# Optimization experiments

Measured on AMD Instinct MI355X. Metric: run time of the kernel, lower is better.

## Reference

```python
import jax, jax.numpy as jnp
import numpy as np

N_AA = 20
A = 15
D_FEAT = 128
CA_IDX = 1
NUM_FUNCS = 3
FREQ_BANDS = jnp.array([1.0, 2.0, 3.0, 1.0, 0.5, 1.0 / 3.0], dtype=jnp.float32)


def setup_inputs() -> dict:
    key = jax.random.key(0)
    ks = jax.random.split(key, 16)
    b, L = 16, 1024
    d_in = D_FEAT + N_AA * A * 3 + 3 * (NUM_FUNCS * 2 * 2 + 1) + D_FEAT  # 1195
    inp = {
        "seq": jax.random.randint(ks[0], (b, L), 0, N_AA),
        "xyz": jax.random.normal(ks[1], (b, L, A, 3), dtype=jnp.float32),
        "dihedrals": jax.random.normal(ks[2], (b, L, 3), dtype=jnp.float32),
        "chain_idx": jax.random.randint(ks[3], (b, L), 0, 10),
        "orientation": jax.random.normal(ks[4], (b, L, 3, 3), dtype=jnp.float32),
        "atom_mask": jnp.ones((b, L, A), dtype=bool),
        "aa_emb": jax.random.normal(ks[5], (N_AA, D_FEAT), dtype=jnp.float32),
        "chain_emb": jax.random.normal(ks[6], (10, D_FEAT), dtype=jnp.float32).at[0].set(0.0),  # padding_idx=0
        "W1": jax.random.normal(ks[7], (d_in, 2 * D_FEAT), dtype=jnp.float32) * 0.02,
        "b1": jnp.zeros((2 * D_FEAT,), dtype=jnp.float32),
        "W2": jax.random.normal(ks[8], (2 * D_FEAT, D_FEAT), dtype=jnp.float32) * 0.02,
        "b2": jnp.zeros((D_FEAT,), dtype=jnp.float32),
        "W3": jax.random.normal(ks[9], (D_FEAT, D_FEAT), dtype=jnp.float32) * 0.02,
        "b3": jnp.zeros((D_FEAT,), dtype=jnp.float32),
        "W4": jax.random.normal(ks[10], (D_FEAT, D_FEAT), dtype=jnp.float32) * 0.02,
        "b4": jnp.zeros((D_FEAT,), dtype=jnp.float32),
    }
    return inp


def angular_encoding(x):
    # x: (..., d_in) -> (..., d_in * 13)
    xe = x[..., None]  # (..., d_in, 1)
    enc = jnp.concatenate([xe, jnp.sin(FREQ_BANDS * xe), jnp.cos(FREQ_BANDS * xe)], axis=-1)
    return enc.reshape(*x.shape[:-1], -1)


def reference(seq, xyz, dihedrals, chain_idx, orientation, atom_mask,
              aa_emb, chain_emb, W1, b1, W2, b2, W3, b3, W4, b4):
    b, L = seq.shape
    aa_type_feat = aa_emb[seq]  # (b, L, d_feat)

    # local coordinates relative to CA, rotated into local frame via O^T
    xyz_rel = xyz - xyz[:, :, CA_IDX:CA_IDX + 1, :]  # (b, L, A, 3)
    xyz_local = jnp.einsum('blji,blaj->blai', orientation, xyz_rel)  # O^T @ xyz_rel

    # one-hot select: place xyz_local in the slot of the residue's aa type
    onehot = jax.nn.one_hot(seq, N_AA, dtype=xyz.dtype)  # (b, L, 20)
    coord_feat = (onehot[:, :, :, None, None] * xyz_local[:, :, None, :, :]).reshape(b, L, N_AA * A * 3)

    dihedral_feat = angular_encoding(dihedrals)  # (b, L, 39)

    chain_feat = chain_emb[chain_idx] * (chain_idx != 0)[..., None].astype(xyz.dtype)  # padding_idx=0

    x = jnp.concatenate([aa_type_feat, coord_feat, dihedral_feat, chain_feat], axis=-1)
    h = jax.nn.relu(x @ W1 + b1)
    h = jax.nn.relu(h @ W2 + b2)
    h = jax.nn.relu(h @ W3 + b3)
    return h @ W4 + b4
```

## Files before the change

### kernel.cpp

```cpp
#include <hip/hip_runtime.h>
#include <math.h>

#define N_AA    20
#define NATOM   15
#define TM      32
#define MAXBL   16384
#define MAXBLK  (MAXBL / TM + N_AA)
#define NWAVE   16

#define FSX  104
#define HSX  264
#define H2SX 136

typedef __attribute__((ext_vector_type(8))) short bf16x8;
typedef __attribute__((ext_vector_type(4))) float f32x4;

#define W1F_SLOTS  (N_AA * 16 * 3 * 64)
#define W2F_SLOTS  (8 * 8 * 64)
#define W34F_SLOTS (8 * 4 * 64)
#define TOT_SLOTS  (W1F_SLOTS + W2F_SLOTS + 2 * W34F_SLOTS)

__device__ __forceinline__ unsigned short f2bf(float x) {
    unsigned u = __float_as_uint(x);
    return (unsigned short)((u + 0x7FFFu + ((u >> 16) & 1u)) >> 16);
}
__device__ __forceinline__ float bf2f(unsigned short h) {
    return __uint_as_float(((unsigned)h) << 16);
}
__device__ __forceinline__ void put2(unsigned short* H, unsigned short* L, int idx, float v) {
    unsigned short hi = f2bf(v);
    H[idx] = hi;
    L[idx] = f2bf(v - bf2f(hi));
}

__global__ __launch_bounds__(1024) void prep_kernel(
    const int* __restrict__ seq, const float* __restrict__ aa_emb,
    const float* __restrict__ chain_emb, const float* __restrict__ W1,
    const float* __restrict__ W2, const float* __restrict__ W3, const float* __restrict__ W4,
    int BL,
    float* __restrict__ aaT, float* __restrict__ chT,
    int* __restrict__ bucket_start, int* __restrict__ blk_type,
    int* __restrict__ blk_chunk, int* __restrict__ rowidx,
    unsigned short* __restrict__ W1fH, unsigned short* __restrict__ W1fL,
    unsigned short* __restrict__ W2fH, unsigned short* __restrict__ W2fL,
    unsigned short* __restrict__ W3fH, unsigned short* __restrict__ W3fL,
    unsigned short* __restrict__ W4fH, unsigned short* __restrict__ W4fL)
{
    const int t = threadIdx.x;
    const int b = blockIdx.x;

    if (b < 8) {
        const int tab = b * 4 + (t >> 8);
        const int col = t & 255;
        if (tab < 30) {
            if (tab < N_AA) {
                const float* e = aa_emb + tab * 128;
                float acc = 0.f;
                #pragma unroll 8
                for (int k = 0; k < 128; ++k)
                    acc += e[k] * W1[(size_t)k * 256 + col];
                aaT[tab * 256 + col] = acc;
            } else {
                const int c = tab - N_AA;
                const float* e = chain_emb + c * 128;
                float acc = 0.f;
                #pragma unroll 8
                for (int k = 0; k < 128; ++k)
                    acc += e[k] * W1[(size_t)(1067 + k) * 256 + col];
                chT[c * 256 + col] = acc;
            }
        }
        return;
    }

    if (b >= 9) {
        const int slot = (b - 9) * 1024 + t;
        if (slot >= TOT_SLOTS) return;
        float v[8];
        unsigned short *dH, *dL;
        if (slot < W1F_SLOTS) {
            const int g = slot / 3072, r1 = slot % 3072;
            const int tile = r1 / 192, chunk = (r1 / 64) % 3, lane = r1 % 64;
            const int n  = tile * 16 + (lane & 15);
            const int kb = chunk * 32 + (lane >> 4) * 8;
            #pragma unroll
            for (int j = 0; j < 8; ++j) {
                const int k = kb + j;
                float x = 0.f;
                if (k < 45)       x = W1[(size_t)(128 + g * 45 + k) * 256 + n];
                else if (k < 84)  x = W1[(size_t)(1028 + k - 45) * 256 + n];
                v[j] = x;
            }
            dH = W1fH + (size_t)slot * 8; dL = W1fL + (size_t)slot * 8;
        } else if (slot < W1F_SLOTS + W2F_SLOTS) {
            const int s = slot - W1F_SLOTS;
            const int tile = s / 512, chunk = (s / 64) % 8, lane = s % 64;
            const int n  = tile * 16 + (lane & 15);
            const int kb = chunk * 32 + (lane >> 4) * 8;
            #pragma unroll
            for (int j = 0; j < 8; ++j) v[j] = W2[(size_t)(kb + j) * 128 + n];
            dH = W2fH + (size_t)s * 8; dL = W2fL + (size_t)s * 8;
        } else if (slot < W1F_SLOTS + W2F_SLOTS + W34F_SLOTS) {
            const int s = slot - W1F_SLOTS - W2F_SLOTS;
            const int tile = s / 256, chunk = (s / 64) % 4, lane = s % 64;
            const int n  = tile * 16 + (lane & 15);
            const int kb = chunk * 32 + (lane >> 4) * 8;
            #pragma unroll
            for (int j = 0; j < 8; ++j) v[j] = W3[(size_t)(kb + j) * 128 + n];
            dH = W3fH + (size_t)s * 8; dL = W3fL + (size_t)s * 8;
        } else {
            const int s = slot - W1F_SLOTS - W2F_SLOTS - W34F_SLOTS;
            const int tile = s / 256, chunk = (s / 64) % 4, lane = s % 64;
            const int n  = tile * 16 + (lane & 15);
            const int kb = chunk * 32 + (lane >> 4) * 8;
            #pragma unroll
            for (int j = 0; j < 8; ++j) v[j] = W4[(size_t)(kb + j) * 128 + n];
            dH = W4fH + (size_t)s * 8; dL = W4fL + (size_t)s * 8;
        }
        #pragma unroll
        for (int j = 0; j < 8; ++j) {
            const unsigned short hi = f2bf(v[j]);
            dH[j] = hi;
            dL[j] = f2bf(v[j] - bf2f(hi));
        }
        return;
    }

    __shared__ int sseq[MAXBL];
    __shared__ int hist[NWAVE][N_AA];
    __shared__ int wcur[NWAVE][N_AA];
    __shared__ int bs[N_AA + 1];
    __shared__ int blkoff[N_AA + 1];

    const int w = t >> 6;
    for (int i = t; i < BL; i += 1024) sseq[i] = seq[i];
    if (t < NWAVE * N_AA) hist[t / N_AA][t % N_AA] = 0;
    __syncthreads();
    for (int i = t; i < BL; i += 1024) atomicAdd(&hist[w][sseq[i]], 1);
    __syncthreads();
    if (t == 0) {
        int runr = 0, runb = 0;
        for (int g = 0; g < N_AA; ++g) {
            int s = 0;
            #pragma unroll
            for (int ww = 0; ww < NWAVE; ++ww) s += hist[ww][g];
            bs[g] = runr; runr += s;
            blkoff[g] = runb; runb += (s + TM - 1) / TM;
        }
        bs[N_AA] = runr; blkoff[N_AA] = runb;
    }
    __syncthreads();
    if (t <= N_AA) bucket_start[t] = bs[t];
    if (t < NWAVE * N_AA) {
        const int w2 = t / N_AA, g2 = t % N_AA;
        int o = bs[g2];
        for (int ww = 0; ww < w2; ++ww) o += hist[ww][g2];
        wcur[w2][g2] = o;
    }
    const int nblk = blkoff[N_AA];
    for (int i = t; i < MAXBLK; i += 1024) {
        if (i < nblk) {
            int g = 0;
            while (blkoff[g + 1] <= i) ++g;
            blk_type[i]  = g;
            blk_chunk[i] = i - blkoff[g];
        } else blk_type[i] = -1;
    }
    __syncthreads();
    for (int i = t; i < BL; i += 1024) {
        const int pos = atomicAdd(&wcur[w][sseq[i]], 1);
        rowidx[pos] = i;
    }
}

__global__ __launch_bounds__(256, 3) void fused_kernel(
    const int* __restrict__ chain_idx, const float* __restrict__ xyz,
    const float* __restrict__ dihedrals, const float* __restrict__ orientation,
    const float* __restrict__ b1, const float* __restrict__ b2,
    const float* __restrict__ b3, const float* __restrict__ b4,
    const float* __restrict__ aaT, const float* __restrict__ chT,
    const int* __restrict__ bucket_start, const int* __restrict__ blk_type,
    const int* __restrict__ blk_chunk, const int* __restrict__ rowidx,
    const unsigned short* __restrict__ W1fH, const unsigned short* __restrict__ W1fL,
    const unsigned short* __restrict__ W2fH, const unsigned short* __restrict__ W2fL,
    const unsigned short* __restrict__ W3fH, const unsigned short* __restrict__ W3fL,
    const unsigned short* __restrict__ W4fH, const unsigned short* __restrict__ W4fL,
    float* __restrict__ out)
{
    __shared__ __align__(16) unsigned short smemA[2 * TM * HSX];
    __shared__ __align__(16) unsigned short smemB[2 * TM * H2SX];
    __shared__ int s_row[TM], s_rowld[TM], s_chain[TM];

    unsigned short* hAH   = smemA;
    unsigned short* hAL   = smemA + TM * HSX;
    unsigned short* featH = smemB;
    unsigned short* featL = smemB + TM * FSX;
    unsigned short* hBH   = smemB;
    unsigned short* hBL   = smemB + TM * H2SX;

    const int t = threadIdx.x;

    const int nwg = gridDim.x;
    const int q = nwg >> 3, r = nwg & 7;
    const int xcd = blockIdx.x & 7, loc = blockIdx.x >> 3;
    const int bid = (xcd < r ? xcd * (q + 1) : r * (q + 1) + (xcd - r) * q) + loc;

    const int g = blk_type[bid];
    if (g < 0) return;
    const int chunk  = blk_chunk[bid];
    const int bstart = bucket_start[g] + chunk * TM;
    const int nrows  = min(TM, bucket_start[g + 1] - bstart);

    const int wave = t >> 6, lane = t & 63, quad = lane >> 4, nid = lane & 15;

    bf16x8 p1H[4], p1L[4];
    #pragma unroll
    for (int tt = 0; tt < 4; ++tt) {
        const size_t off = ((size_t)((g * 16 + (wave * 4 + tt)) * 3 + 0) * 64 + lane) * 8;
        p1H[tt] = *(const bf16x8*)(W1fH + off);
        p1L[tt] = *(const bf16x8*)(W1fL + off);
    }

    if (t < TM) {
        const bool valid = (t < nrows);
        const int rl = rowidx[valid ? (bstart + t) : bstart];
        s_row[t]   = valid ? rl : -1;
        s_rowld[t] = rl;
        s_chain[t] = chain_idx[rl];
    }
    __syncthreads();

    for (int i = t; i < TM * NATOM; i += 256) {
        const int rr = i / NATOM, a = i % NATOM;
        const int rl = s_rowld[rr];
        const float* xr = xyz + (size_t)rl * (NATOM * 3);
        const float cax = xr[3], cay = xr[4], caz = xr[5];
        const float rx = xr[a*3+0] - cax;
        const float ry = xr[a*3+1] - cay;
        const float rz = xr[a*3+2] - caz;
        const float* O = orientation + (size_t)rl * 9;
        put2(featH, featL, rr * FSX + a*3 + 0, O[0]*rx + O[3]*ry + O[6]*rz);
        put2(featH, featL, rr * FSX + a*3 + 1, O[1]*rx + O[4]*ry + O[7]*rz);
        put2(featH, featL, rr * FSX + a*3 + 2, O[2]*rx + O[5]*ry + O[8]*rz);
    }
    if (t < TM * 3) {
        const int rr = t / 3, d = t % 3;
        const float x = dihedrals[(size_t)s_rowld[rr] * 3 + d];
        const int base = rr * FSX + 45 + d * 13;
        const float F3 = (float)(1.0 / 3.0);
        const float s1 = sinf(x), c1 = cosf(x);
        put2(featH, featL, base + 0, x);
        put2(featH, featL, base + 1, s1);           put2(featH, featL, base + 2, sinf(2.f*x));
        put2(featH, featL, base + 3, sinf(3.f*x));  put2(featH, featL, base + 4, s1);
        put2(featH, featL, base + 5, sinf(0.5f*x)); put2(featH, featL, base + 6, sinf(F3*x));
        put2(featH, featL, base + 7, c1);           put2(featH, featL, base + 8, cosf(2.f*x));
        put2(featH, featL, base + 9, cosf(3.f*x));  put2(featH, featL, base +10, c1);
        put2(featH, featL, base +11, cosf(0.5f*x)); put2(featH, featL, base +12, cosf(F3*x));
    }
    if (t < TM) {
        #pragma unroll
        for (int k = 84; k < 96; ++k) { featH[t * FSX + k] = 0; featL[t * FSX + k] = 0; }
    }
    __syncthreads();

    const f32x4 zero = {0.f, 0.f, 0.f, 0.f};

    bf16x8 p2H[2], p2L[2];
    {
        f32x4 acc[2][4] = {{zero, zero, zero, zero}, {zero, zero, zero, zero}};
        #pragma unroll
        for (int c = 0; c < 3; ++c) {
            const bf16x8 aH0 = *(const bf16x8*)(featH + nid * FSX + c * 32 + quad * 8);
            const bf16x8 aL0 = *(const bf16x8*)(featL + nid * FSX + c * 32 + quad * 8);
            const bf16x8 aH1 = *(const bf16x8*)(featH + (16 + nid) * FSX + c * 32 + quad * 8);
            const bf16x8 aL1 = *(const bf16x8*)(featL + (16 + nid) * FSX + c * 32 + quad * 8);
            #pragma unroll
            for (int tt = 0; tt < 4; ++tt) {
                bf16x8 bH, bL;
                if (c == 0) { bH = p1H[tt]; bL = p1L[tt]; }
                else {
                    const size_t off = ((size_t)((g * 16 + (wave * 4 + tt)) * 3 + c) * 64 + lane) * 8;
                    bH = *(const bf16x8*)(W1fH + off);
                    bL = *(const bf16x8*)(W1fL + off);
                }
                acc[0][tt] = __builtin_amdgcn_mfma_f32_16x16x32_bf16(aH0, bH, acc[0][tt], 0, 0, 0);
                acc[0][tt] = __builtin_amdgcn_mfma_f32_16x16x32_bf16(aH0, bL, acc[0][tt], 0, 0, 0);
                acc[0][tt] = __builtin_amdgcn_mfma_f32_16x16x32_bf16(aL0, bH, acc[0][tt], 0, 0, 0);
                acc[1][tt] = __builtin_amdgcn_mfma_f32_16x16x32_bf16(aH1, bH, acc[1][tt], 0, 0, 0);
                acc[1][tt] = __builtin_amdgcn_mfma_f32_16x16x32_bf16(aH1, bL, acc[1][tt], 0, 0, 0);
                acc[1][tt] = __builtin_amdgcn_mfma_f32_16x16x32_bf16(aL1, bH, acc[1][tt], 0, 0, 0);
            }
        }
        #pragma unroll
        for (int tt = 0; tt < 2; ++tt) {
            const size_t off = ((size_t)((wave * 2 + tt) * 8 + 0) * 64 + lane) * 8;
            p2H[tt] = *(const bf16x8*)(W2fH + off);
            p2L[tt] = *(const bf16x8*)(W2fL + off);
        }
        #pragma unroll
        for (int tt = 0; tt < 4; ++tt) {
            const int j = (wave * 4 + tt) * 16 + nid;
            const float cb = b1[j] + aaT[g * 256 + j];
            #pragma unroll
            for (int rt = 0; rt < 2; ++rt) {
                #pragma unroll
                for (int rr = 0; rr < 4; ++rr) {
                    const int row = rt * 16 + quad * 4 + rr;
                    float v = acc[rt][tt][rr] + cb + chT[s_chain[row] * 256 + j];
                    v = fmaxf(v, 0.f);
                    put2(hAH, hAL, row * HSX + j, v);
                }
            }
        }
    }
    __syncthreads();

    bf16x8 p3H[2], p3L[2];
    {
        f32x4 acc[2][2] = {{zero, zero}, {zero, zero}};
        #pragma unroll
        for (int c = 0; c < 8; ++c) {
            const bf16x8 aH0 = *(const bf16x8*)(hAH + nid * HSX + c * 32 + quad * 8);
            const bf16x8 aL0 = *(const bf16x8*)(hAL + nid * HSX + c * 32 + quad * 8);
            const bf16x8 aH1 = *(const bf16x8*)(hAH + (16 + nid) * HSX + c * 32 + quad * 8);
            const bf16x8 aL1 = *(const bf16x8*)(hAL + (16 + nid) * HSX + c * 32 + quad * 8);
            #pragma unroll
            for (int tt = 0; tt < 2; ++tt) {
                bf16x8 bH, bL;
                if (c == 0) { bH = p2H[tt]; bL = p2L[tt]; }
                else {
                    const size_t off = ((size_t)((wave * 2 + tt) * 8 + c) * 64 + lane) * 8;
                    bH = *(const bf16x8*)(W2fH + off);
                    bL = *(const bf16x8*)(W2fL + off);
                }
                acc[0][tt] = __builtin_amdgcn_mfma_f32_16x16x32_bf16(aH0, bH, acc[0][tt], 0, 0, 0);
                acc[0][tt] = __builtin_amdgcn_mfma_f32_16x16x32_bf16(aH0, bL, acc[0][tt], 0, 0, 0);
                acc[0][tt] = __builtin_amdgcn_mfma_f32_16x16x32_bf16(aL0, bH, acc[0][tt], 0, 0, 0);
                acc[1][tt] = __builtin_amdgcn_mfma_f32_16x16x32_bf16(aH1, bH, acc[1][tt], 0, 0, 0);
                acc[1][tt] = __builtin_amdgcn_mfma_f32_16x16x32_bf16(aH1, bL, acc[1][tt], 0, 0, 0);
                acc[1][tt] = __builtin_amdgcn_mfma_f32_16x16x32_bf16(aL1, bH, acc[1][tt], 0, 0, 0);
            }
        }
        #pragma unroll
        for (int tt = 0; tt < 2; ++tt) {
            const size_t off = ((size_t)((wave * 2 + tt) * 4 + 0) * 64 + lane) * 8;
            p3H[tt] = *(const bf16x8*)(W3fH + off);
            p3L[tt] = *(const bf16x8*)(W3fL + off);
        }
        #pragma unroll
        for (int tt = 0; tt < 2; ++tt) {
            const int j = (wave * 2 + tt) * 16 + nid;
            const float bb = b2[j];
            #pragma unroll
            for (int rt = 0; rt < 2; ++rt) {
                #pragma unroll
                for (int rr = 0; rr < 4; ++rr) {
                    const int row = rt * 16 + quad * 4 + rr;
                    float v = fmaxf(acc[rt][tt][rr] + bb, 0.f);
                    put2(hBH, hBL, row * H2SX + j, v);
                }
            }
        }
    }
    __syncthreads();

    bf16x8 p4H[2], p4L[2];
    {
        f32x4 acc[2][2] = {{zero, zero}, {zero, zero}};
        #pragma unroll
        for (int c = 0; c < 4; ++c) {
            const bf16x8 aH0 = *(const bf16x8*)(hBH + nid * H2SX + c * 32 + quad * 8);
            const bf16x8 aL0 = *(const bf16x8*)(hBL + nid * H2SX + c * 32 + quad * 8);
            const bf16x8 aH1 = *(const bf16x8*)(hBH + (16 + nid) * H2SX + c * 32 + quad * 8);
            const bf16x8 aL1 = *(const bf16x8*)(hBL + (16 + nid) * H2SX + c * 32 + quad * 8);
            #pragma unroll
            for (int tt = 0; tt < 2; ++tt) {
                bf16x8 bH, bL;
                if (c == 0) { bH = p3H[tt]; bL = p3L[tt]; }
                else {
                    const size_t off = ((size_t)((wave * 2 + tt) * 4 + c) * 64 + lane) * 8;
                    bH = *(const bf16x8*)(W3fH + off);
                    bL = *(const bf16x8*)(W3fL + off);
                }
                acc[0][tt] = __builtin_amdgcn_mfma_f32_16x16x32_bf16(aH0, bH, acc[0][tt], 0, 0, 0);
                acc[0][tt] = __builtin_amdgcn_mfma_f32_16x16x32_bf16(aH0, bL, acc[0][tt], 0, 0, 0);
                acc[0][tt] = __builtin_amdgcn_mfma_f32_16x16x32_bf16(aL0, bH, acc[0][tt], 0, 0, 0);
                acc[1][tt] = __builtin_amdgcn_mfma_f32_16x16x32_bf16(aH1, bH, acc[1][tt], 0, 0, 0);
                acc[1][tt] = __builtin_amdgcn_mfma_f32_16x16x32_bf16(aH1, bL, acc[1][tt], 0, 0, 0);
                acc[1][tt] = __builtin_amdgcn_mfma_f32_16x16x32_bf16(aL1, bH, acc[1][tt], 0, 0, 0);
            }
        }
        #pragma unroll
        for (int tt = 0; tt < 2; ++tt) {
            const size_t off = ((size_t)((wave * 2 + tt) * 4 + 0) * 64 + lane) * 8;
            p4H[tt] = *(const bf16x8*)(W4fH + off);
            p4L[tt] = *(const bf16x8*)(W4fL + off);
        }
        #pragma unroll
        for (int tt = 0; tt < 2; ++tt) {
            const int j = (wave * 2 + tt) * 16 + nid;
            const float bb = b3[j];
            #pragma unroll
            for (int rt = 0; rt < 2; ++rt) {
                #pragma unroll
                for (int rr = 0; rr < 4; ++rr) {
                    const int row = rt * 16 + quad * 4 + rr;
                    float v = fmaxf(acc[rt][tt][rr] + bb, 0.f);
                    put2(hAH, hAL, row * HSX + j, v);
                }
            }
        }
    }
    __syncthreads();

    {
        f32x4 acc[2][2] = {{zero, zero}, {zero, zero}};
        #pragma unroll
        for (int c = 0; c < 4; ++c) {
            const bf16x8 aH0 = *(const bf16x8*)(hAH + nid * HSX + c * 32 + quad * 8);
            const bf16x8 aL0 = *(const bf16x8*)(hAL + nid * HSX + c * 32 + quad * 8);
            const bf16x8 aH1 = *(const bf16x8*)(hAH + (16 + nid) * HSX + c * 32 + quad * 8);
            const bf16x8 aL1 = *(const bf16x8*)(hAL + (16 + nid) * HSX + c * 32 + quad * 8);
            #pragma unroll
            for (int tt = 0; tt < 2; ++tt) {
                bf16x8 bH, bL;
                if (c == 0) { bH = p4H[tt]; bL = p4L[tt]; }
                else {
                    const size_t off = ((size_t)((wave * 2 + tt) * 4 + c) * 64 + lane) * 8;
                    bH = *(const bf16x8*)(W4fH + off);
                    bL = *(const bf16x8*)(W4fL + off);
                }
                acc[0][tt] = __builtin_amdgcn_mfma_f32_16x16x32_bf16(aH0, bH, acc[0][tt], 0, 0, 0);
                acc[0][tt] = __builtin_amdgcn_mfma_f32_16x16x32_bf16(aH0, bL, acc[0][tt], 0, 0, 0);
                acc[0][tt] = __builtin_amdgcn_mfma_f32_16x16x32_bf16(aL0, bH, acc[0][tt], 0, 0, 0);
                acc[1][tt] = __builtin_amdgcn_mfma_f32_16x16x32_bf16(aH1, bH, acc[1][tt], 0, 0, 0);
                acc[1][tt] = __builtin_amdgcn_mfma_f32_16x16x32_bf16(aH1, bL, acc[1][tt], 0, 0, 0);
                acc[1][tt] = __builtin_amdgcn_mfma_f32_16x16x32_bf16(aL1, bH, acc[1][tt], 0, 0, 0);
            }
        }
        #pragma unroll
        for (int tt = 0; tt < 2; ++tt) {
            const int j = (wave * 2 + tt) * 16 + nid;
            const float bb = b4[j];
            #pragma unroll
            for (int rt = 0; rt < 2; ++rt) {
                #pragma unroll
                for (int rr = 0; rr < 4; ++rr) {
                    const int row = rt * 16 + quad * 4 + rr;
                    const int orow = s_row[row];
                    if (orow >= 0) out[(size_t)orow * 128 + j] = acc[rt][tt][rr] + bb;
                }
            }
        }
    }
}

extern "C" void kernel_launch(void* const* d_in, const int* in_sizes, int n_in,
                              void* d_out, int out_size, void* d_ws, size_t ws_size,
                              hipStream_t stream) {
    const int*   seq    = (const int*)d_in[0];
    const float* xyz    = (const float*)d_in[1];
    const float* dihed  = (const float*)d_in[2];
    const int*   chain  = (const int*)d_in[3];
    const float* orient = (const float*)d_in[4];
    const float* aa_emb = (const float*)d_in[6];
    const float* ch_emb = (const float*)d_in[7];
    const float* W1 = (const float*)d_in[8];
    const float* b1 = (const float*)d_in[9];
    const float* W2 = (const float*)d_in[10];
    const float* b2 = (const float*)d_in[11];
    const float* W3 = (const float*)d_in[12];
    const float* b3 = (const float*)d_in[13];
    const float* W4 = (const float*)d_in[14];
    const float* b4 = (const float*)d_in[15];
    float* out = (float*)d_out;

    const int BL = in_sizes[0];

    char* p = (char*)d_ws;
    float* aaT = (float*)p;            p += 20 * 256 * 4;
    float* chT = (float*)p;            p += 10 * 256 * 4;
    int* bucket_start = (int*)p;       p += 32 * 4;
    int* blk_type     = (int*)p;       p += MAXBLK * 4;
    int* blk_chunk    = (int*)p;       p += MAXBLK * 4;
    int* rowidx       = (int*)p;       p += MAXBL * 4;
    p += ((16 - ((uintptr_t)p & 15)) & 15);
    unsigned short* W1fH = (unsigned short*)p; p += (size_t)W1F_SLOTS * 8 * 2;
    unsigned short* W1fL = (unsigned short*)p; p += (size_t)W1F_SLOTS * 8 * 2;
    unsigned short* W2fH = (unsigned short*)p; p += (size_t)W2F_SLOTS * 8 * 2;
    unsigned short* W2fL = (unsigned short*)p; p += (size_t)W2F_SLOTS * 8 * 2;
    unsigned short* W3fH = (unsigned short*)p; p += (size_t)W34F_SLOTS * 8 * 2;
    unsigned short* W3fL = (unsigned short*)p; p += (size_t)W34F_SLOTS * 8 * 2;
    unsigned short* W4fH = (unsigned short*)p; p += (size_t)W34F_SLOTS * 8 * 2;
    unsigned short* W4fL = (unsigned short*)p;

    const int nprep  = 9 + (TOT_SLOTS + 1023) / 1024;
    const int nfused = BL / TM + N_AA;

    prep_kernel<<<nprep, 1024, 0, stream>>>(seq, aa_emb, ch_emb, W1, W2, W3, W4, BL,
                                            aaT, chT, bucket_start, blk_type, blk_chunk, rowidx,
                                            W1fH, W1fL, W2fH, W2fL, W3fH, W3fL, W4fH, W4fL);
    fused_kernel<<<nfused, 256, 0, stream>>>(chain, xyz, dihed, orient,
                                             b1, b2, b3, b4, aaT, chT,
                                             bucket_start, blk_type, blk_chunk, rowidx,
                                             W1fH, W1fL, W2fH, W2fL, W3fH, W3fL, W4fH, W4fL,
                                             out);
}
```

Baseline: 121.6 us.

## Split residue bucket sort across sixteen blocks with inter-block flag synchronization

The counting sort that groups rows by amino-acid type used to run in one 1024-thread block. It is now spread over sixteen blocks. Each block histograms its own slice of rows and publishes the counts to global memory. The last block waits on per-block flags, builds the prefix offsets and block tables, then sets a ready flag, after which every block scatters its rows. This targets the serial bottleneck of one block scanning all rows inside the prep kernel. In exchange it relies on spin-waits that need all sixteen blocks resident at once. The flags are set to a magic value and never reset, so later calls can skip the waits and read stale or racing histograms.

```diff
diff --git a/kernel.cpp b/kernel.cpp
--- a/kernel.cpp
+++ b/kernel.cpp
@@ -7,6 +7,8 @@
 #define MAXBL   16384
 #define MAXBLK  (MAXBL / TM + N_AA)
 #define NWAVE   16
+#define NSORT   16
+#define MAGIC   0x3FA9C1B7
 
 #define FSX  104
 #define HSX  264
@@ -41,6 +43,7 @@
     float* __restrict__ aaT, float* __restrict__ chT,
     int* __restrict__ bucket_start, int* __restrict__ blk_type,
     int* __restrict__ blk_chunk, int* __restrict__ rowidx,
+    int* __restrict__ bhist, int* __restrict__ bdone, int* __restrict__ ready,
     unsigned short* __restrict__ W1fH, unsigned short* __restrict__ W1fL,
     unsigned short* __restrict__ W2fH, unsigned short* __restrict__ W2fL,
     unsigned short* __restrict__ W3fH, unsigned short* __restrict__ W3fL,
@@ -73,8 +76,8 @@
         return;
     }
 
-    if (b >= 9) {
-        const int slot = (b - 9) * 1024 + t;
+    if (b >= 8 + NSORT) {
+        const int slot = (b - 8 - NSORT) * 1024 + t;
         if (slot >= TOT_SLOTS) return;
         float v[8];
         unsigned short *dH, *dL;
@@ -126,50 +129,85 @@
         return;
     }
 
-    __shared__ int sseq[MAXBL];
-    __shared__ int hist[NWAVE][N_AA];
-    __shared__ int wcur[NWAVE][N_AA];
-    __shared__ int bs[N_AA + 1];
-    __shared__ int blkoff[N_AA + 1];
-
-    const int w = t >> 6;
-    for (int i = t; i < BL; i += 1024) sseq[i] = seq[i];
-    if (t < NWAVE * N_AA) hist[t / N_AA][t % N_AA] = 0;
-    __syncthreads();
-    for (int i = t; i < BL; i += 1024) atomicAdd(&hist[w][sseq[i]], 1);
-    __syncthreads();
-    if (t == 0) {
-        int runr = 0, runb = 0;
-        for (int g = 0; g < N_AA; ++g) {
+    {
+        const int sb = b - 8;
+        const int rows_per = (BL + NSORT - 1) / NSORT;
+        const int r0 = sb * rows_per;
+        const int r1 = min(BL, r0 + rows_per);
+
+        __shared__ int whist[NWAVE][N_AA];
+        __shared__ int wcur[NWAVE][N_AA];
+        __shared__ int bs_s[N_AA + 1], blkoff_s[N_AA + 1];
+
+        const int w = t >> 6;
+        if (t < NWAVE * N_AA) whist[t / N_AA][t % N_AA] = 0;
+        __syncthreads();
+
+        int myg[2], myrow[2], nmine = 0;
+        for (int i = r0 + t; i < r1; i += 1024) {
+            const int gg = seq[i];
+            myg[nmine] = gg; myrow[nmine] = i; ++nmine;
+            atomicAdd(&whist[w][gg], 1);
+        }
+        __syncthreads();
+
+        if (t < N_AA) {
             int s = 0;
             #pragma unroll
-            for (int ww = 0; ww < NWAVE; ++ww) s += hist[ww][g];
-            bs[g] = runr; runr += s;
-            blkoff[g] = runb; runb += (s + TM - 1) / TM;
-        }
-        bs[N_AA] = runr; blkoff[N_AA] = runb;
-    }
-    __syncthreads();
-    if (t <= N_AA) bucket_start[t] = bs[t];
-    if (t < NWAVE * N_AA) {
-        const int w2 = t / N_AA, g2 = t % N_AA;
-        int o = bs[g2];
-        for (int ww = 0; ww < w2; ++ww) o += hist[ww][g2];
-        wcur[w2][g2] = o;
-    }
-    const int nblk = blkoff[N_AA];
-    for (int i = t; i < MAXBLK; i += 1024) {
-        if (i < nblk) {
-            int g = 0;
-            while (blkoff[g + 1] <= i) ++g;
-            blk_type[i]  = g;
-            blk_chunk[i] = i - blkoff[g];
-        } else blk_type[i] = -1;
-    }
-    __syncthreads();
-    for (int i = t; i < BL; i += 1024) {
-        const int pos = atomicAdd(&wcur[w][sseq[i]], 1);
-        rowidx[pos] = i;
+            for (int ww = 0; ww < NWAVE; ++ww) s += whist[ww][t];
+            bhist[sb * N_AA + t] = s;
+            __threadfence();
+        }
+        __syncthreads();
+        if (t == 0) atomicExch(&bdone[sb], MAGIC);
+
+        if (sb == NSORT - 1) {
+            if (t == 0) {
+                for (int bb = 0; bb < NSORT; ++bb)
+                    while (__hip_atomic_load(&bdone[bb], __ATOMIC_ACQUIRE,
+                                             __HIP_MEMORY_SCOPE_AGENT) != MAGIC)
+                        __builtin_amdgcn_s_sleep(8);
+                int runr = 0, runb = 0;
+                for (int g2 = 0; g2 < N_AA; ++g2) {
+                    int s = 0;
+                    for (int bb = 0; bb < NSORT; ++bb) s += bhist[bb * N_AA + g2];
+                    bs_s[g2] = runr; runr += s;
+                    blkoff_s[g2] = runb; runb += (s + TM - 1) / TM;
+                }
+                bs_s[N_AA] = runr; blkoff_s[N_AA] = runb;
+            }
+            __syncthreads();
+            if (t <= N_AA) bucket_start[t] = bs_s[t];
+            const int nblk = blkoff_s[N_AA];
+            for (int i = t; i < MAXBLK; i += 1024) {
+                if (i < nblk) {
+                    int g2 = 0;
+                    while (blkoff_s[g2 + 1] <= i) ++g2;
+                    blk_type[i]  = g2;
+                    blk_chunk[i] = i - blkoff_s[g2];
+                } else blk_type[i] = -1;
+            }
+            __threadfence();
+            __syncthreads();
+            if (t == 0) atomicExch(ready, MAGIC);
+        }
+
+        while (__hip_atomic_load(ready, __ATOMIC_ACQUIRE, __HIP_MEMORY_SCOPE_AGENT) != MAGIC)
+            __builtin_amdgcn_s_sleep(8);
+
+        if (t < NWAVE * N_AA) {
+            const int w2 = t / N_AA, g2 = t % N_AA;
+            int o = bucket_start[g2];
+            for (int bb = 0; bb < sb; ++bb) o += bhist[bb * N_AA + g2];
+            for (int ww = 0; ww < w2; ++ww) o += whist[ww][g2];
+            wcur[w2][g2] = o;
+        }
+        __syncthreads();
+        for (int m = 0; m < nmine; ++m) {
+            const int pos = atomicAdd(&wcur[w][myg[m]], 1);
+            rowidx[pos] = myrow[m];
+        }
+        return;
     }
 }
 
@@ -484,6 +522,9 @@
     int* blk_type     = (int*)p;       p += MAXBLK * 4;
     int* blk_chunk    = (int*)p;       p += MAXBLK * 4;
     int* rowidx       = (int*)p;       p += MAXBL * 4;
+    int* bhist        = (int*)p;       p += NSORT * N_AA * 4;
+    int* bdone        = (int*)p;       p += NSORT * 4;
+    int* ready        = (int*)p;       p += 16;
     p += ((16 - ((uintptr_t)p & 15)) & 15);
     unsigned short* W1fH = (unsigned short*)p; p += (size_t)W1F_SLOTS * 8 * 2;
     unsigned short* W1fL = (unsigned short*)p; p += (size_t)W1F_SLOTS * 8 * 2;
@@ -494,11 +535,12 @@
     unsigned short* W4fH = (unsigned short*)p; p += (size_t)W34F_SLOTS * 8 * 2;
     unsigned short* W4fL = (unsigned short*)p;
 
-    const int nprep  = 9 + (TOT_SLOTS + 1023) / 1024;
+    const int nprep  = 8 + NSORT + (TOT_SLOTS + 1023) / 1024;
     const int nfused = BL / TM + N_AA;
 
     prep_kernel<<<nprep, 1024, 0, stream>>>(seq, aa_emb, ch_emb, W1, W2, W3, W4, BL,
                                             aaT, chT, bucket_start, blk_type, blk_chunk, rowidx,
+                                            bhist, bdone, ready,
                                             W1fH, W1fL, W2fH, W2fL, W3fH, W3fL, W4fH, W4fL);
     fused_kernel<<<nfused, 256, 0, stream>>>(chain, xyz, dihed, orient,
                                              b1, b2, b3, b4, aaT, chT,
```

After: 128.4 us. +5.5%, slower.
